# Kernel tuning notes

Measured on AMD Instinct MI355X. Metric: run time of the kernel, lower is better.

Reference implementation:

```python
import jax, jax.numpy as jnp
import numpy as np

EPS = 1e-5

def _conv3x3(x, w, b):
    # x: (B,C,H,W), w: (O,I,3,3) OIHW, SAME padding, stride 1
    y = jax.lax.conv_general_dilated(x, w, (1, 1), 'SAME',
                                     dimension_numbers=('NCHW', 'OIHW', 'NCHW'))
    return y + b[None, :, None, None]

def _inorm(x):
    # InstanceNorm2d (affine=False, eval-free): per-sample per-channel over HW
    m = jnp.mean(x, axis=(2, 3), keepdims=True)
    v = jnp.var(x, axis=(2, 3), keepdims=True)
    return (x - m) * jax.lax.rsqrt(v + EPS)

def _pac_conv_transpose(x, guide, w, b, stride=2, padding=1, out_pad=1):
    # PacConvTranspose2d (gaussian kernel, not channel-wise, unnormalized):
    # 1) zero-stuff input by stride, pad by (k-1)-padding (+output_padding on the
    #    bottom/right), 2) run a 3x3 conv whose taps are modulated per-pixel by
    #    K_ij = exp(-0.5 * ||g(p+ij) - g(p)||^2) computed from the guidance map.
    # w: (Cin, Cout, k, k)  (torch transposed-conv layout)
    k = w.shape[2]
    B, C, H, Wd = x.shape
    xs = jnp.zeros((B, C, (H - 1) * stride + 1, (Wd - 1) * stride + 1), x.dtype)
    xs = xs.at[:, :, ::stride, ::stride].set(x)
    p = (k - 1) - padding
    xp = jnp.pad(xs, ((0, 0), (0, 0), (p, p + out_pad), (p, p + out_pad)))
    gpad = (k - 1) // 2
    gp = jnp.pad(guide, ((0, 0), (0, 0), (gpad, gpad), (gpad, gpad)))
    Ho, Wo = guide.shape[2], guide.shape[3]
    out = jnp.zeros((B, w.shape[1], Ho, Wo), x.dtype)
    for i in range(k):          # fixed 3x3 tap loop (not a data-dim loop)
        for j in range(k):
            gn = gp[:, :, i:i + Ho, j:j + Wo]
            kk = jnp.exp(-0.5 * jnp.sum((gn - guide) ** 2, axis=1, keepdims=True))  # (B,1,Ho,Wo)
            xn = xp[:, :, i:i + Ho, j:j + Wo]                                        # (B,Cin,Ho,Wo)
            out = out + jnp.einsum('bchw,co->bohw', xn * kk, w[:, :, i, j])
    return out + b[None, :, None, None]

def setup_inputs() -> dict:
    key = jax.random.key(0)
    ks = jax.random.split(key, 16)
    C = 64
    s = 0.02  # small weight scale to keep gaussian adaptive kernels well-conditioned
    inp = {
        'x':      jax.random.normal(ks[0], (1, 4 * C, 64, 64), jnp.float32),
        'ef_lv2': jax.random.normal(ks[1], (1, 2 * C, 128, 128), jnp.float32),
        'ef_lv1': jax.random.normal(ks[2], (1, C, 256, 256), jnp.float32),
        'w_adj2': jax.random.normal(ks[3], (4 * C, 2 * C, 3, 3), jnp.float32) * s,
        'b_adj2': jnp.zeros((4 * C,), jnp.float32),
        'w_adj1': jax.random.normal(ks[4], (2 * C, C, 3, 3), jnp.float32) * s,
        'b_adj1': jnp.zeros((2 * C,), jnp.float32),
        'w_pac16': jax.random.normal(ks[5], (4 * C, 2 * C, 3, 3), jnp.float32) * s,
        'b_pac16': jnp.zeros((2 * C,), jnp.float32),
        'w_pac20': jax.random.normal(ks[6], (2 * C, C, 3, 3), jnp.float32) * s,
        'b_pac20': jnp.zeros((C,), jnp.float32),
        'w_out':  jax.random.normal(ks[7], (3, C, 3, 3), jnp.float32) * s,
        'b_out':  jnp.zeros((3,), jnp.float32),
    }
    return inp

def reference(x, ef_lv2, ef_lv1, w_adj2, b_adj2, w_adj1, b_adj1,
              w_pac16, b_pac16, w_pac20, b_pac20, w_out, b_out):
    x = _inorm(x) + x                       # layer13 + residual
    x = _inorm(x) + x                       # layer14 + residual
    g2 = _conv3x3(ef_lv2, w_adj2, b_adj2)   # adjust_ef_lv2_pacconv
    x = _pac_conv_transpose(x, g2, w_pac16, b_pac16)  # layer16: 64->128
    x = _inorm(x) + x                       # layer17
    x = _inorm(x) + x                       # layer18
    g1 = _conv3x3(ef_lv1, w_adj1, b_adj1)   # adjust_ef_lv1_pacconv
    x = _pac_conv_transpose(x, g1, w_pac20, b_pac20)  # layer20: 128->256
    x = _inorm(x) + x                       # layer21
    x = _inorm(x) + x                       # layer22
    return _conv3x3(x, w_out, b_out)        # layer24 -> (B,3,256,256)
```

## Files before the change

### kernel.cpp

```cpp
#include <hip/hip_runtime.h>
#include <hip/hip_bf16.h>
#include <cstdint>
#include <cstddef>

#define EPS_IN 1e-5f

typedef __attribute__((ext_vector_type(8))) short short8;
typedef __attribute__((ext_vector_type(4))) float floatx4;
typedef __attribute__((ext_vector_type(8))) unsigned short ushort8;
typedef __attribute__((ext_vector_type(4))) unsigned int uint4v;
typedef __attribute__((address_space(3))) unsigned int lds_uint;
typedef __attribute__((address_space(1))) const unsigned int glb_uint;

__device__ __forceinline__ unsigned short f2bf(float f) {
    unsigned int u = __float_as_uint(f);
    u += 0x7FFFu + ((u >> 16) & 1u);
    return (unsigned short)(u >> 16);
}
__device__ __forceinline__ float bf2f(unsigned short s) {
    return __uint_as_float((unsigned int)s << 16);
}
__device__ __forceinline__ float bflo(unsigned int u) {
    return __uint_as_float(u << 16);
}
__device__ __forceinline__ float bfhi(unsigned int u) {
    return __uint_as_float(u & 0xFFFF0000u);
}

__device__ __forceinline__ void composed_norm(float s, float q, float HW,
                                              float& A, float& B) {
    float m1 = s / HW;
    float v1 = q / HW - m1 * m1;
    float r1 = rsqrtf(v1 + EPS_IN);
    float a1 = 1.f + r1;
    float b1 = -m1 * r1;
    float r2 = rsqrtf(a1 * a1 * v1 + EPS_IN);
    float a2 = 1.f + r2;
    A = a1 * a2;
    B = a2 * b1 - m1 * r2;
}

__device__ __forceinline__ void border_zero(unsigned short* buf, int C, int H, int W, int idx) {
    int Hp = H + 2, Wp = W + 2;
    int cg8 = C >> 3;
    int cg = idx % cg8;
    int bi = idx / cg8;
    int y, x;
    if (bi < Wp) { y = 0; x = bi; }
    else if (bi < 2 * Wp) { y = Hp - 1; x = bi - Wp; }
    else {
        int k = bi - 2 * Wp;
        y = 1 + (k >> 1);
        x = (k & 1) ? (Wp - 1) : 0;
    }
    ushort8 z = {0, 0, 0, 0, 0, 0, 0, 0};
    *(ushort8*)&buf[((size_t)y * Wp + x) * C + cg * 8] = z;
}

__device__ __forceinline__ void reorder_one(const float* w, unsigned short* dst,
                                            int O, int C, int j) {
    int cg8 = C >> 3;
    int cg = j % cg8;
    int o = (j / cg8) % O;
    int tap = j / (cg8 * O);
    ushort8 v;
#pragma unroll
    for (int i = 0; i < 8; i++)
        v[i] = f2bf(w[((size_t)o * C + cg * 8 + i) * 9 + tap]);
    *(ushort8*)&dst[((size_t)tap * O + o) * C + cg * 8] = v;
}
__device__ __forceinline__ void stack_one(const float* w, unsigned short* dst,
                                          int C, int O, int j) {
    int cg8 = C >> 3;
    int cg = j % cg8;
    int o = (j / cg8) % O;
    int tap = j / (cg8 * O);
    ushort8 v;
#pragma unroll
    for (int i = 0; i < 8; i++)
        v[i] = f2bf(w[((size_t)(cg * 8 + i) * O + o) * 9 + tap]);
    *(ushort8*)&dst[((size_t)tap * O + o) * C + cg * 8] = v;
}

__device__ __forceinline__ void pad_one(const float* in, unsigned short* xp,
                                        int C, int H, int W, int t) {
    int HW = H * W;
    int p = t % HW;
    int cg = t / HW;
    int y = p / W, x = p % W;
    ushort8 v;
#pragma unroll
    for (int i = 0; i < 8; i++)
        v[i] = f2bf(in[(size_t)(cg * 8 + i) * HW + p]);
    *(ushort8*)&xp[((size_t)(y + 1) * (W + 2) + (x + 1)) * C + cg * 8] = v;
}

__global__ void prologue_kernel(uint4v* __restrict__ statz,
                                unsigned short* __restrict__ xp2,
                                unsigned short* __restrict__ xp1,
                                const float* __restrict__ w_adj2, unsigned short* __restrict__ Wr2,
                                const float* __restrict__ w_adj1, unsigned short* __restrict__ Wr1,
                                const float* __restrict__ w_p16, unsigned short* __restrict__ Wt16,
                                const float* __restrict__ w_p20, unsigned short* __restrict__ Wt20,
                                const float* __restrict__ ef2, const float* __restrict__ ef1,
                                const float* __restrict__ x, float2* __restrict__ statX) {
    __shared__ float ss[4], sq[4];
    int b = blockIdx.x;
    if (b < 68) {
        int t = b * 256 + threadIdx.x;
        const int NZ = 864;
        const int N2 = 516 * 16;
        const int N1 = 1028 * 8;
        if (t < NZ) {
            uint4v z = {0u, 0u, 0u, 0u};
            statz[t] = z;
        } else if (t < NZ + N2) {
            border_zero(xp2, 128, 128, 128, t - NZ);
        } else if (t < NZ + N2 + N1) {
            border_zero(xp1, 64, 256, 256, t - NZ - N2);
        }
    } else if (b < 428) {
        int t = (b - 68) * 256 + threadIdx.x;
        if (t < 36864) reorder_one(w_adj2, Wr2, 256, 128, t);
        else if (t < 46080) reorder_one(w_adj1, Wr1, 128, 64, t - 36864);
        else if (t < 82944) stack_one(w_p16, Wt16, 256, 128, t - 46080);
        else if (t < 92160) stack_one(w_p20, Wt20, 128, 64, t - 82944);
    } else if (b < 3500) {
        int t = (b - 428) * 256 + threadIdx.x;
        if (t < 262144) pad_one(ef2, xp2, 128, 128, 128, t);
        else            pad_one(ef1, xp1, 64, 256, 256, t - 262144);
    } else {
        int c = b - 3500;
        const float* src = x + (size_t)c * 4096;
        float s = 0.f, q = 0.f;
#pragma unroll
        for (int k = 0; k < 4; k++) {
            float4 v = *(const float4*)(src + k * 1024 + threadIdx.x * 4);
            s += v.x + v.y + v.z + v.w;
            q += v.x * v.x + v.y * v.y + v.z * v.z + v.w * v.w;
        }
#pragma unroll
        for (int off = 32; off >= 1; off >>= 1) {
            s += __shfl_down(s, off, 64);
            q += __shfl_down(q, off, 64);
        }
        int wave = threadIdx.x >> 6;
        if ((threadIdx.x & 63) == 0) { ss[wave] = s; sq[wave] = q; }
        __syncthreads();
        if (threadIdx.x == 0) {
            float2 o;
            o.x = ss[0] + ss[1] + ss[2] + ss[3];
            o.y = sq[0] + sq[1] + sq[2] + sq[3];
            statX[c] = o;
        }
    }
}

template <int CIN>
__device__ void conv3x3_body(const unsigned short* __restrict__ xp,
                             const unsigned short* __restrict__ wre,
                             const float* __restrict__ bias,
                             unsigned short* __restrict__ gpl,
                             int O, int H, int W, int bx) {
    __shared__ short Bbuf[390 * 32];
    __shared__ short Abuf[3 * 128 * 32];
    int tid = threadIdx.x;
    int lane = tid & 63, wid = tid >> 6;
    int mi = wid >> 1, ni = wid & 1;
    int l15 = lane & 15, khi = lane >> 4;
    int tpr = W >> 7;
    int y = bx / tpr;
    int x0 = (bx % tpr) << 7;
    int o0 = 0;
    int Wp = W + 2;
    int HW = H * W;

    floatx4 acc[4][4];
#pragma unroll
    for (int sm = 0; sm < 4; sm++)
#pragma unroll
        for (int r = 0; r < 4; r++) {
            float bv = bias[o0 + mi * 64 + sm * 16 + khi * 4 + r];
#pragma unroll
            for (int sn = 0; sn < 4; sn++) acc[sm][sn][r] = bv;
        }

    for (int cc = 0; cc < CIN / 32; cc++) {
        __syncthreads();
#pragma unroll
        for (int k = 0; k < 7; k++) {
            int s = k * 256 + tid;
            if (s < 1560) {
                int r = s >> 2, q = s & 3;
                int dy = r / 130, col = r % 130;
                const unsigned short* g =
                    xp + ((size_t)(y + dy) * Wp + x0 + col) * CIN + cc * 32 + q * 8;
                __builtin_amdgcn_global_load_lds((glb_uint*)g, (lds_uint*)(Bbuf + s * 8), 16, 0, 0);
            }
        }
        for (int dy = 0; dy < 3; dy++) {
            __syncthreads();
#pragma unroll
            for (int k = 0; k < 6; k++) {
                int s = k * 256 + tid;
                int dx = s >> 9, m = (s >> 2) & 127, q = s & 3;
                const unsigned short* g =
                    wre + ((size_t)((dy * 3 + dx) * O + o0 + m)) * CIN + cc * 32 + q * 8;
                __builtin_amdgcn_global_load_lds((glb_uint*)g, (lds_uint*)(Abuf + s * 8), 16, 0, 0);
            }
            __syncthreads();
#pragma unroll
            for (int dx = 0; dx < 3; dx++) {
                short8 a[4], b[4];
#pragma unroll
                for (int sm = 0; sm < 4; sm++)
                    a[sm] = *(const short8*)&Abuf[(dx * 128 + mi * 64 + sm * 16 + l15) * 32 + khi * 8];
#pragma unroll
                for (int sn = 0; sn < 4; sn++)
                    b[sn] = *(const short8*)&Bbuf[(dy * 130 + ni * 64 + sn * 16 + l15 + dx) * 32 + khi * 8];
#pragma unroll
                for (int sm = 0; sm < 4; sm++)
#pragma unroll
                    for (int sn = 0; sn < 4; sn++)
                        acc[sm][sn] = __builtin_amdgcn_mfma_f32_16x16x32_bf16(
                            a[sm], b[sn], acc[sm][sn], 0, 0, 0);
            }
        }
    }
#pragma unroll
    for (int sm = 0; sm < 4; sm++)
#pragma unroll
        for (int sn = 0; sn < 4; sn++) {
            int ob = o0 + mi * 64 + sm * 16 + khi * 4;
            int px = x0 + ni * 64 + sn * 16 + l15;
#pragma unroll
            for (int r = 0; r < 4; r++)
                gpl[(size_t)(ob + r) * HW + (size_t)y * W + px] = f2bf(acc[sm][sn][r]);
        }
}

template <int CIN>
__launch_bounds__(256, 1)
__global__ void conv3x3_mfma_at_kernel(const unsigned short* __restrict__ xp,
                                       const unsigned short* __restrict__ wre,
                                       const float* __restrict__ bias,
                                       unsigned short* __restrict__ gpl,
                                       int O, int H, int W) {
    __shared__ short Bbuf[390 * 32];
    __shared__ short Abuf[9 * 128 * 32];
    int tid = threadIdx.x;
    int lane = tid & 63, wid = tid >> 6;
    int mi = wid >> 1, ni = wid & 1;
    int l15 = lane & 15, khi = lane >> 4;
    int tpr = W >> 7;
    int y = blockIdx.x / tpr;
    int x0 = (blockIdx.x % tpr) << 7;
    int o0 = blockIdx.y << 7;
    int Wp = W + 2;
    int HW = H * W;

    floatx4 acc[4][4];
#pragma unroll
    for (int sm = 0; sm < 4; sm++)
#pragma unroll
        for (int r = 0; r < 4; r++) {
            float bv = bias[o0 + mi * 64 + sm * 16 + khi * 4 + r];
#pragma unroll
            for (int sn = 0; sn < 4; sn++) acc[sm][sn][r] = bv;
        }

    for (int cc = 0; cc < CIN / 32; cc++) {
        __syncthreads();
#pragma unroll
        for (int k = 0; k < 7; k++) {
            int s = k * 256 + tid;
            if (s < 1560) {
                int r = s >> 2, q = s & 3;
                int dy = r / 130, col = r % 130;
                const unsigned short* g =
                    xp + ((size_t)(y + dy) * Wp + x0 + col) * CIN + cc * 32 + q * 8;
                __builtin_amdgcn_global_load_lds((glb_uint*)g, (lds_uint*)(Bbuf + s * 8), 16, 0, 0);
            }
        }
#pragma unroll
        for (int k = 0; k < 18; k++) {
            int s = k * 256 + tid;
            int row = s >> 2, q = s & 3;
            int tap = row >> 7, m = row & 127;
            const unsigned short* g =
                wre + ((size_t)(tap * O + o0 + m)) * CIN + cc * 32 + q * 8;
            __builtin_amdgcn_global_load_lds((glb_uint*)g, (lds_uint*)(Abuf + s * 8), 16, 0, 0);
        }
        __syncthreads();
#pragma unroll
        for (int dy = 0; dy < 3; dy++)
#pragma unroll
            for (int dx = 0; dx < 3; dx++) {
                short8 a[4], b[4];
#pragma unroll
                for (int sm = 0; sm < 4; sm++)
                    a[sm] = *(const short8*)&Abuf[((dy * 3 + dx) * 128 + mi * 64 + sm * 16 + l15) * 32 + khi * 8];
#pragma unroll
                for (int sn = 0; sn < 4; sn++)
                    b[sn] = *(const short8*)&Bbuf[(dy * 130 + ni * 64 + sn * 16 + l15 + dx) * 32 + khi * 8];
#pragma unroll
                for (int sm = 0; sm < 4; sm++)
#pragma unroll
                    for (int sn = 0; sn < 4; sn++)
                        acc[sm][sn] = __builtin_amdgcn_mfma_f32_16x16x32_bf16(
                            a[sm], b[sn], acc[sm][sn], 0, 0, 0);
            }
    }
#pragma unroll
    for (int sm = 0; sm < 4; sm++)
#pragma unroll
        for (int sn = 0; sn < 4; sn++) {
            int ob = o0 + mi * 64 + sm * 16 + khi * 4;
            int px = x0 + ni * 64 + sn * 16 + l15;
#pragma unroll
            for (int r = 0; r < 4; r++)
                gpl[(size_t)(ob + r) * HW + (size_t)y * W + px] = f2bf(acc[sm][sn][r]);
        }
}

template <int CC>
__device__ __forceinline__ void kk_part_body(const unsigned short* __restrict__ g,
                                             float* __restrict__ S,
                                             int H, int W, int c0, int idx) {
    int Wh = W >> 1;
    int y = idx / Wh, xs = idx % Wh;
    int HW = H * W, HW4 = HW >> 2;
    int ys = y >> 1, ry = y & 1;
    bool xg = (xs + 1 < Wh);
    int off2 = xg ? 1 : 0;
    const unsigned short* gy = g + (size_t)y * W + 2 * xs + (size_t)c0 * HW;
    int slot = ys * Wh + xs;

    if (ry == 0) {
        float s3 = 0.f, s5 = 0.f;
        for (int c = 0; c < CC; c++) {
            const unsigned int* p = (const unsigned int*)(gy + (size_t)c * HW);
            unsigned int cc = p[0];
            unsigned int n2 = p[off2];
            float ce = bflo(cc), co = bfhi(cc);
            float d3 = ce - co;
            float d5 = bflo(n2) - co;
            s3 += d3 * d3;
            s5 += d5 * d5;
        }
        S[(size_t)3 * HW4 + slot] = s3;
        S[(size_t)4 * HW4 + slot] = 0.f;
        S[(size_t)5 * HW4 + slot] = xg ? s5 : 0.f;
    } else {
        bool yg = (y + 1 < H);
        float s0 = 0.f, s1 = 0.f, s2 = 0.f, s6 = 0.f, s7 = 0.f, s8 = 0.f;
        if (yg) {
            for (int c = 0; c < CC; c++) {
                const unsigned int* pc = (const unsigned int*)(gy + (size_t)c * HW);
                const unsigned int* pm = (const unsigned int*)(gy - W + (size_t)c * HW);
                const unsigned int* pp = (const unsigned int*)(gy + W + (size_t)c * HW);
                unsigned int cc = pc[0];
                unsigned int m0 = pm[0], m2 = pm[off2];
                unsigned int q0 = pp[0], q2 = pp[off2];
                float ce = bflo(cc), co = bfhi(cc);
                float nm = bflo(m0), np = bflo(q0);
                float d1 = nm - ce, d0 = nm - co, d2 = bflo(m2) - co;
                float d7 = np - ce, d6 = np - co, d8 = bflo(q2) - co;
                s1 += d1 * d1; s0 += d0 * d0; s2 += d2 * d2;
                s7 += d7 * d7; s6 += d6 * d6; s8 += d8 * d8;
            }
        } else {
            for (int c = 0; c < CC; c++) {
                const unsigned int* pc = (const unsigned int*)(gy + (size_t)c * HW);
                const unsigned int* pm = (const unsigned int*)(gy - W + (size_t)c * HW);
                unsigned int cc = pc[0];
                unsigned int m0 = pm[0], m2 = pm[off2];
                float ce = bflo(cc), co = bfhi(cc);
                float nm = bflo(m0);
                float d1 = nm - ce, d0 = nm - co, d2 = bflo(m2) - co;
                s1 += d1 * d1; s0 += d0 * d0; s2 += d2 * d2;
            }
        }
        S[(size_t)0 * HW4 + slot] = s0;
        S[(size_t)1 * HW4 + slot] = s1;
        S[(size_t)2 * HW4 + slot] = xg ? s2 : 0.f;
        S[(size_t)6 * HW4 + slot] = s6;
        S[(size_t)7 * HW4 + slot] = s7;
        S[(size_t)8 * HW4 + slot] = (xg && yg) ? s8 : 0.f;
    }
}

__launch_bounds__(256, 2)
__global__ void convg1_kk2_kernel(const unsigned short* __restrict__ Xp1,
                                  const unsigned short* __restrict__ Wr1,
                                  const float* __restrict__ b_adj1,
                                  unsigned short* __restrict__ Gp1,
                                  const unsigned short* __restrict__ Gp2,
                                  float* __restrict__ Sp2) {
    int b = blockIdx.x;
    if (b < 512) {
        conv3x3_body<64>(Xp1, Wr1, b_adj1, Gp1, 128, 256, 256, b);
    } else {
        b -= 512;
        int chunk = b >> 5, xblk = b & 31;
        kk_part_body<16>(Gp2, Sp2 + (size_t)chunk * 9 * 4096, 128, 128,
                         chunk * 16, xblk * 256 + (int)threadIdx.x);
    }
}

__global__ void kk1_red2_transpose_kernel(const unsigned short* __restrict__ Gp1,
                                          float* __restrict__ Sp1,
                                          const float* __restrict__ Sp2, float* __restrict__ Sf2,
                                          const float* __restrict__ x,
                                          const float2* __restrict__ statX,
                                          unsigned short* __restrict__ Xt16) {
    int b = blockIdx.x;
    if (b < 1024) {
        int chunk = b >> 7, xblk = b & 127;
        kk_part_body<16>(Gp1, Sp1 + (size_t)chunk * 9 * 16384, 256, 256,
                         chunk * 16, xblk * 256 + (int)threadIdx.x);
    } else if (b < 1168) {
        int i = (b - 1024) * 256 + threadIdx.x;
        if (i < 36864) {
            float s = 0.f;
            for (int ch = 0; ch < 16; ch++) s += Sp2[(size_t)ch * 36864 + i];
            Sf2[i] = s;
        }
    } else {
        int t = (b - 1168) * 256 + threadIdx.x;
        int p = t % 4096;
        int cg = t / 4096;
        float Av[8], Bv[8];
#pragma unroll
        for (int i = 0; i < 8; i++) {
            float2 pp = statX[cg * 8 + i];
            composed_norm(pp.x, pp.y, 4096.f, Av[i], Bv[i]);
        }
        ushort8 v;
#pragma unroll
        for (int i = 0; i < 8; i++) {
            float xv = x[(size_t)(cg * 8 + i) * 4096 + p];
            v[i] = f2bf(fmaf(xv, Av[i], Bv[i]));
        }
        *(ushort8*)&Xt16[(size_t)p * 256 + cg * 8] = v;
    }
}

template <int K>
__device__ void gemm_bt_body(const unsigned short* __restrict__ A,
                             const unsigned short* __restrict__ B,
                             unsigned short* __restrict__ P, int N,
                             int m0, int n0) {
    __shared__ short Ab[128 * 32];
    __shared__ short Bb[128 * 32];
    int tid = threadIdx.x;
    int lane = tid & 63, wid = tid >> 6;
    int mi = wid >> 1, ni = wid & 1;
    int l15 = lane & 15, khi = lane >> 4;

    floatx4 acc[4][4];
#pragma unroll
    for (int sm = 0; sm < 4; sm++)
#pragma unroll
        for (int sn = 0; sn < 4; sn++)
#pragma unroll
            for (int r = 0; r < 4; r++) acc[sm][sn][r] = 0.f;

    for (int kc = 0; kc < K / 32; kc++) {
        __syncthreads();
#pragma unroll
        for (int k = 0; k < 2; k++) {
            int s = k * 256 + tid;
            int row = s >> 2, q = s & 3;
            const unsigned short* ga = A + (size_t)(m0 + row) * K + kc * 32 + q * 8;
            __builtin_amdgcn_global_load_lds((glb_uint*)ga, (lds_uint*)(Ab + s * 8), 16, 0, 0);
            const unsigned short* gb = B + (size_t)(n0 + row) * K + kc * 32 + q * 8;
            __builtin_amdgcn_global_load_lds((glb_uint*)gb, (lds_uint*)(Bb + s * 8), 16, 0, 0);
        }
        __syncthreads();
        short8 a[4], b[4];
#pragma unroll
        for (int sm = 0; sm < 4; sm++)
            a[sm] = *(const short8*)&Ab[(mi * 64 + sm * 16 + l15) * 32 + khi * 8];
#pragma unroll
        for (int sn = 0; sn < 4; sn++)
            b[sn] = *(const short8*)&Bb[(ni * 64 + sn * 16 + l15) * 32 + khi * 8];
#pragma unroll
        for (int sm = 0; sm < 4; sm++)
#pragma unroll
            for (int sn = 0; sn < 4; sn++)
                acc[sm][sn] = __builtin_amdgcn_mfma_f32_16x16x32_bf16(
                    a[sm], b[sn], acc[sm][sn], 0, 0, 0);
    }
#pragma unroll
    for (int sm = 0; sm < 4; sm++)
#pragma unroll
        for (int sn = 0; sn < 4; sn++) {
            int m = m0 + mi * 64 + sm * 16 + khi * 4;
            int n = n0 + ni * 64 + sn * 16 + l15;
#pragma unroll
            for (int r = 0; r < 4; r++)
                P[(size_t)(m + r) * N + n] = f2bf(acc[sm][sn][r]);
        }
}

__launch_bounds__(256, 3)
__global__ void gemm16_red1_kernel(const unsigned short* __restrict__ Wt16,
                                   const unsigned short* __restrict__ Xt16,
                                   unsigned short* __restrict__ P16,
                                   const float* __restrict__ Sp1, float* __restrict__ Sf1) {
    int b = blockIdx.x;
    if (b < 288) {
        int n0 = (b & 31) << 7;
        int m0 = (b >> 5) << 7;
        gemm_bt_body<256>(Wt16, Xt16, P16, 4096, m0, n0);
    } else {
        int i = (b - 288) * 256 + threadIdx.x;
        if (i < 147456) {
            float s = 0.f;
            for (int ch = 0; ch < 8; ch++) s += Sp1[(size_t)ch * 147456 + i];
            Sf1[i] = s;
        }
    }
}

template <int K>
__launch_bounds__(256, 3)
__global__ void gemm_bt_kernel(const unsigned short* __restrict__ A,
                               const unsigned short* __restrict__ B,
                               unsigned short* __restrict__ P, int N) {
    gemm_bt_body<K>(A, B, P, N, blockIdx.y << 7, blockIdx.x << 7);
}

__global__ void transpose_norm2_bf16_kernel(const unsigned short* __restrict__ in,
                                            const float2* __restrict__ parts, int NB,
                                            unsigned short* __restrict__ xt,
                                            int C, int HW) {
    int t = blockIdx.x * blockDim.x + threadIdx.x;
    int p = t % HW;
    int cg = t / HW;
    float Av[8], Bv[8];
#pragma unroll
    for (int i = 0; i < 8; i++) {
        int c = cg * 8 + i;
        float s = 0.f, q = 0.f;
        for (int nb = 0; nb < NB; nb++) {
            float2 pp = parts[c * NB + nb];
            s += pp.x; q += pp.y;
        }
        composed_norm(s, q, (float)HW, Av[i], Bv[i]);
    }
    ushort8 v;
#pragma unroll
    for (int i = 0; i < 8; i++) {
        float x = bf2f(in[(size_t)(cg * 8 + i) * HW + p]);
        v[i] = f2bf(fmaf(x, Av[i], Bv[i]));
    }
    *(ushort8*)&xt[(size_t)p * C + cg * 8] = v;
}

__global__ void pac_combine2_kernel(const unsigned short* __restrict__ P,
                                    const float* __restrict__ S,
                                    const float* __restrict__ bias,
                                    unsigned short* __restrict__ out,
                                    float2* __restrict__ statOut,
                                    int O, int Hi, int Wi) {
    int HW4 = Hi * Wi;
    int Wo = Wi * 2;
    int HoWo = 4 * HW4;
    int idx = blockIdx.x * blockDim.x + threadIdx.x;
    int pixh = idx % HW4;
    int og = idx / HW4;
    int ys = pixh / Wi, xs = pixh % Wi;
    int ry = blockIdx.z;
    int y = 2 * ys + ry;
    bool xg = (xs + 1 < Wi);
    bool yg = (ys + 1 < Hi);
    size_t rowb = (size_t)ys * Wi + xs;

    float ev[4], ov[4];

    if (ry == 0) {
        float k3 = __expf(-0.5f * S[(size_t)3 * HW4 + pixh]);
        float k4 = __expf(-0.5f * S[(size_t)4 * HW4 + pixh]);
        float k5 = __expf(-0.5f * S[(size_t)5 * HW4 + pixh]);
#pragma unroll
        for (int r = 0; r < 4; r++) {
            int o = og * 4 + r;
            float bv = bias[o];
            const unsigned short* p3 = P + (size_t)(3 * O + o) * HW4 + rowb;
            const unsigned short* p4 = P + (size_t)(4 * O + o) * HW4 + rowb;
            const unsigned short* p5 = P + (size_t)(5 * O + o) * HW4 + rowb;
            float v4 = bf2f(p4[0]);
            float v3 = bf2f(p3[0]);
            float v5 = xg ? bf2f(p5[1]) : 0.f;
            ev[r] = bv + k4 * v4;
            ov[r] = bv + k3 * v3 + k5 * v5;
        }
    } else {
        float k0 = __expf(-0.5f * S[(size_t)0 * HW4 + pixh]);
        float k1 = __expf(-0.5f * S[(size_t)1 * HW4 + pixh]);
        float k2 = __expf(-0.5f * S[(size_t)2 * HW4 + pixh]);
        float k6 = __expf(-0.5f * S[(size_t)6 * HW4 + pixh]);
        float k7 = __expf(-0.5f * S[(size_t)7 * HW4 + pixh]);
        float k8 = __expf(-0.5f * S[(size_t)8 * HW4 + pixh]);
#pragma unroll
        for (int r = 0; r < 4; r++) {
            int o = og * 4 + r;
            float bv = bias[o];
            const unsigned short* p0 = P + (size_t)(0 * O + o) * HW4 + rowb;
            const unsigned short* p1 = P + (size_t)(1 * O + o) * HW4 + rowb;
            const unsigned short* p2 = P + (size_t)(2 * O + o) * HW4 + rowb;
            const unsigned short* p6 = P + (size_t)(6 * O + o) * HW4 + rowb + Wi;
            const unsigned short* p7 = P + (size_t)(7 * O + o) * HW4 + rowb + Wi;
            const unsigned short* p8 = P + (size_t)(8 * O + o) * HW4 + rowb + Wi;
            float v1 = bf2f(p1[0]);
            float v0 = bf2f(p0[0]);
            float v2 = xg ? bf2f(p2[1]) : 0.f;
            float v7 = yg ? bf2f(p7[0]) : 0.f;
            float v6 = yg ? bf2f(p6[0]) : 0.f;
            float v8 = (yg && xg) ? bf2f(p8[1]) : 0.f;
            ev[r] = bv + k1 * v1 + k7 * v7;
            ov[r] = bv + k0 * v0 + k2 * v2 + k6 * v6 + k8 * v8;
        }
    }
#pragma unroll
    for (int r = 0; r < 4; r++) {
        unsigned int pk = (unsigned int)f2bf(ev[r]) | ((unsigned int)f2bf(ov[r]) << 16);
        *(unsigned int*)&out[(size_t)(og * 4 + r) * HoWo + (size_t)y * Wo + 2 * xs] = pk;
    }

    __shared__ float rs[4][4], rq[4][4];
    int wave = threadIdx.x >> 6;
#pragma unroll
    for (int r = 0; r < 4; r++) {
        float s = ev[r] + ov[r];
        float q = ev[r] * ev[r] + ov[r] * ov[r];
#pragma unroll
        for (int off = 32; off >= 1; off >>= 1) {
            s += __shfl_down(s, off, 64);
            q += __shfl_down(q, off, 64);
        }
        if ((threadIdx.x & 63) == 0) { rs[wave][r] = s; rq[wave][r] = q; }
    }
    __syncthreads();
    if (threadIdx.x < 4) {
        int r = threadIdx.x;
        float s = rs[0][r] + rs[1][r] + rs[2][r] + rs[3][r];
        float q = rq[0][r] + rq[1][r] + rq[2][r] + rq[3][r];
        atomicAdd(&statOut[og * 4 + r].x, s);
        atomicAdd(&statOut[og * 4 + r].y, q);
    }
}

__global__ void conv_part_norm_kernel(const unsigned short* __restrict__ in,
                                      const float* __restrict__ w,
                                      const float2* __restrict__ parts, int NB,
                                      float* __restrict__ Pf, int H, int W) {
    __shared__ float wsm[16 * 9 * 3];
    __shared__ float am[16], bm[16];
    int q0 = blockIdx.y * 16;
    int HW = H * W;
    for (int t = threadIdx.x; t < 432; t += blockDim.x) {
        int oc = t % 3;
        int tap = (t / 3) % 9;
        int c = t / 27;
        wsm[t] = w[((size_t)oc * 64 + q0 + c) * 9 + tap];
    }
    if (threadIdx.x < 16) {
        int c = q0 + threadIdx.x;
        float s = 0.f, q = 0.f;
        for (int nb = 0; nb < NB; nb++) {
            float2 pp = parts[c * NB + nb];
            s += pp.x; q += pp.y;
        }
        float A, B;
        composed_norm(s, q, (float)HW, A, B);
        am[threadIdx.x] = A;
        bm[threadIdx.x] = B;
    }
    __syncthreads();
    int pix = blockIdx.x * blockDim.x + threadIdx.x;
    int y = pix / W, x = pix % W;
    float acc[3] = {0.f, 0.f, 0.f};
    bool xl = (x > 0), xr = (x < W - 1);
    for (int c = 0; c < 16; c++) {
        const unsigned short* base = in + (size_t)(q0 + c) * HW + pix;
        const float* wc = wsm + c * 27;
        float ac = am[c], bc = bm[c];
#pragma unroll
        for (int dy = 0; dy < 3; dy++) {
            int yy = y + dy - 1;
            if (yy < 0 || yy >= H) continue;
            const unsigned short* row = base + (dy - 1) * W;
            float v0 = xl ? fmaf(bf2f(row[-1]), ac, bc) : 0.f;
            float v1 = fmaf(bf2f(row[0]), ac, bc);
            float v2 = xr ? fmaf(bf2f(row[1]), ac, bc) : 0.f;
#pragma unroll
            for (int ob = 0; ob < 3; ob++) {
                acc[ob] += v0 * wc[(dy * 3 + 0) * 3 + ob];
                acc[ob] += v1 * wc[(dy * 3 + 1) * 3 + ob];
                acc[ob] += v2 * wc[(dy * 3 + 2) * 3 + ob];
            }
        }
    }
#pragma unroll
    for (int ob = 0; ob < 3; ob++)
        Pf[(size_t)(blockIdx.y * 3 + ob) * HW + pix] = acc[ob];
}

__global__ void conv_fin_kernel(const float* __restrict__ Pf, const float* __restrict__ bias,
                                float* __restrict__ out, int HW) {
    int pix = blockIdx.x * blockDim.x + threadIdx.x;
#pragma unroll
    for (int ob = 0; ob < 3; ob++) {
        float a = bias[ob];
#pragma unroll
        for (int q = 0; q < 4; q++)
            a += Pf[(size_t)(q * 3 + ob) * HW + pix];
        out[(size_t)ob * HW + pix] = a;
    }
}

extern "C" void kernel_launch(void* const* d_in, const int* in_sizes, int n_in,
                              void* d_out, int out_size, void* d_ws, size_t ws_size,
                              hipStream_t stream) {
    const float* x      = (const float*)d_in[0];
    const float* ef2    = (const float*)d_in[1];
    const float* ef1    = (const float*)d_in[2];
    const float* w_adj2 = (const float*)d_in[3];
    const float* b_adj2 = (const float*)d_in[4];
    const float* w_adj1 = (const float*)d_in[5];
    const float* b_adj1 = (const float*)d_in[6];
    const float* w_p16  = (const float*)d_in[7];
    const float* b_p16  = (const float*)d_in[8];
    const float* w_p20  = (const float*)d_in[9];
    const float* b_p20  = (const float*)d_in[10];
    const float* w_out  = (const float*)d_in[11];
    const float* b_out  = (const float*)d_in[12];
    float* out = (float*)d_out;

    float* ws = (float*)d_ws;
    unsigned short* bxb1 = (unsigned short*)(ws + 1048576);
    unsigned short* bxb2 = (unsigned short*)(ws + 3145728);
    unsigned short* Wt16 = (unsigned short*)(ws + 5242880);
    unsigned short* Xt16 = (unsigned short*)(ws + 5390336);
    float* bk2c = ws + 7340032;
    float* bk1c = ws + 7376896;
    float2* statX   = (float2*)(ws + 7524352);
    float2* statP16 = (float2*)(ws + 7525376);
    float2* statP20 = (float2*)(ws + 7526656);
    unsigned short* Wt20 = (unsigned short*)(ws + 7528832);
    unsigned short* Gp1  = (unsigned short*)(ws + 7569792);
    unsigned short* P16  = (unsigned short*)(ws + 7569792);
    unsigned short* P20  = (unsigned short*)(ws + 7569792);
    unsigned short* Gp2  = (unsigned short*)(ws + 12812672);
    unsigned short* Xt20 = (unsigned short*)(ws + 12812672);
    unsigned short* Xp2 = (unsigned short*)(ws + 14975872);
    unsigned short* Wr2 = (unsigned short*)(ws + 16057472);
    unsigned short* Xp1 = (unsigned short*)(ws + 16204928);
    unsigned short* Wr1 = (unsigned short*)(ws + 18334976);
    float* Pf = ws + 14975872;
    float* Sp2 = ws + 18371840;
    float* Sp1 = ws + 18961664;

    prologue_kernel<<<3756, 256, 0, stream>>>(
        (uint4v*)(ws + 7525376), Xp2, Xp1,
        w_adj2, Wr2, w_adj1, Wr1, w_p16, Wt16, w_p20, Wt20,
        ef2, ef1, x, statX);

    conv3x3_mfma_at_kernel<128><<<dim3(128, 2), 256, 0, stream>>>(Xp2, Wr2, b_adj2, Gp2, 256, 128, 128);

    convg1_kk2_kernel<<<1024, 256, 0, stream>>>(Xp1, Wr1, b_adj1, Gp1, Gp2, Sp2);

    kk1_red2_transpose_kernel<<<1680, 256, 0, stream>>>(Gp1, Sp1, Sp2, bk2c, x, statX, Xt16);

    gemm16_red1_kernel<<<864, 256, 0, stream>>>(Wt16, Xt16, P16, Sp1, bk1c);

    pac_combine2_kernel<<<dim3(512, 1, 2), 256, 0, stream>>>(P16, bk2c, b_p16, bxb1, statP16, 128, 64, 64);

    transpose_norm2_bf16_kernel<<<1024, 256, 0, stream>>>(bxb1, statP16, 1, Xt20, 128, 16384);

    gemm_bt_kernel<128><<<dim3(128, 5), 256, 0, stream>>>(Wt20, Xt20, P20, 16384);

    pac_combine2_kernel<<<dim3(1024, 1, 2), 256, 0, stream>>>(P20, bk1c, b_p20, bxb2, statP20, 64, 128, 128);

    conv_part_norm_kernel<<<dim3(256, 4), 256, 0, stream>>>(bxb2, w_out, statP20, 1, Pf, 256, 256);
    conv_fin_kernel<<<256, 256, 0, stream>>>(Pf, b_out, out, 65536);
}
```

Baseline: 234.1 us.

## Run g1 guide conv with the all-taps conv kernel and regroup the kk and reduction stages

```diff
diff --git a/kernel.cpp b/kernel.cpp
--- a/kernel.cpp
+++ b/kernel.cpp
@@ -154,89 +154,6 @@
             statX[c] = o;
         }
     }
-}
-
-template <int CIN>
-__device__ void conv3x3_body(const unsigned short* __restrict__ xp,
-                             const unsigned short* __restrict__ wre,
-                             const float* __restrict__ bias,
-                             unsigned short* __restrict__ gpl,
-                             int O, int H, int W, int bx) {
-    __shared__ short Bbuf[390 * 32];
-    __shared__ short Abuf[3 * 128 * 32];
-    int tid = threadIdx.x;
-    int lane = tid & 63, wid = tid >> 6;
-    int mi = wid >> 1, ni = wid & 1;
-    int l15 = lane & 15, khi = lane >> 4;
-    int tpr = W >> 7;
-    int y = bx / tpr;
-    int x0 = (bx % tpr) << 7;
-    int o0 = 0;
-    int Wp = W + 2;
-    int HW = H * W;
-
-    floatx4 acc[4][4];
-#pragma unroll
-    for (int sm = 0; sm < 4; sm++)
-#pragma unroll
-        for (int r = 0; r < 4; r++) {
-            float bv = bias[o0 + mi * 64 + sm * 16 + khi * 4 + r];
-#pragma unroll
-            for (int sn = 0; sn < 4; sn++) acc[sm][sn][r] = bv;
-        }
-
-    for (int cc = 0; cc < CIN / 32; cc++) {
-        __syncthreads();
-#pragma unroll
-        for (int k = 0; k < 7; k++) {
-            int s = k * 256 + tid;
-            if (s < 1560) {
-                int r = s >> 2, q = s & 3;
-                int dy = r / 130, col = r % 130;
-                const unsigned short* g =
-                    xp + ((size_t)(y + dy) * Wp + x0 + col) * CIN + cc * 32 + q * 8;
-                __builtin_amdgcn_global_load_lds((glb_uint*)g, (lds_uint*)(Bbuf + s * 8), 16, 0, 0);
-            }
-        }
-        for (int dy = 0; dy < 3; dy++) {
-            __syncthreads();
-#pragma unroll
-            for (int k = 0; k < 6; k++) {
-                int s = k * 256 + tid;
-                int dx = s >> 9, m = (s >> 2) & 127, q = s & 3;
-                const unsigned short* g =
-                    wre + ((size_t)((dy * 3 + dx) * O + o0 + m)) * CIN + cc * 32 + q * 8;
-                __builtin_amdgcn_global_load_lds((glb_uint*)g, (lds_uint*)(Abuf + s * 8), 16, 0, 0);
-            }
-            __syncthreads();
-#pragma unroll
-            for (int dx = 0; dx < 3; dx++) {
-                short8 a[4], b[4];
-#pragma unroll
-                for (int sm = 0; sm < 4; sm++)
-                    a[sm] = *(const short8*)&Abuf[(dx * 128 + mi * 64 + sm * 16 + l15) * 32 + khi * 8];
-#pragma unroll
-                for (int sn = 0; sn < 4; sn++)
-                    b[sn] = *(const short8*)&Bbuf[(dy * 130 + ni * 64 + sn * 16 + l15 + dx) * 32 + khi * 8];
-#pragma unroll
-                for (int sm = 0; sm < 4; sm++)
-#pragma unroll
-                    for (int sn = 0; sn < 4; sn++)
-                        acc[sm][sn] = __builtin_amdgcn_mfma_f32_16x16x32_bf16(
-                            a[sm], b[sn], acc[sm][sn], 0, 0, 0);
-            }
-        }
-    }
-#pragma unroll
-    for (int sm = 0; sm < 4; sm++)
-#pragma unroll
-        for (int sn = 0; sn < 4; sn++) {
-            int ob = o0 + mi * 64 + sm * 16 + khi * 4;
-            int px = x0 + ni * 64 + sn * 16 + l15;
-#pragma unroll
-            for (int r = 0; r < 4; r++)
-                gpl[(size_t)(ob + r) * HW + (size_t)y * W + px] = f2bf(acc[sm][sn][r]);
-        }
 }
 
 template <int CIN>
@@ -390,44 +307,25 @@
     }
 }
 
-__launch_bounds__(256, 2)
-__global__ void convg1_kk2_kernel(const unsigned short* __restrict__ Xp1,
-                                  const unsigned short* __restrict__ Wr1,
-                                  const float* __restrict__ b_adj1,
-                                  unsigned short* __restrict__ Gp1,
-                                  const unsigned short* __restrict__ Gp2,
-                                  float* __restrict__ Sp2) {
+__global__ void kk_both_transpose_kernel(const unsigned short* __restrict__ Gp2,
+                                         float* __restrict__ Sp2,
+                                         const unsigned short* __restrict__ Gp1,
+                                         float* __restrict__ Sp1,
+                                         const float* __restrict__ x,
+                                         const float2* __restrict__ statX,
+                                         unsigned short* __restrict__ Xt16) {
     int b = blockIdx.x;
     if (b < 512) {
-        conv3x3_body<64>(Xp1, Wr1, b_adj1, Gp1, 128, 256, 256, b);
-    } else {
-        b -= 512;
         int chunk = b >> 5, xblk = b & 31;
         kk_part_body<16>(Gp2, Sp2 + (size_t)chunk * 9 * 4096, 128, 128,
                          chunk * 16, xblk * 256 + (int)threadIdx.x);
-    }
-}
-
-__global__ void kk1_red2_transpose_kernel(const unsigned short* __restrict__ Gp1,
-                                          float* __restrict__ Sp1,
-                                          const float* __restrict__ Sp2, float* __restrict__ Sf2,
-                                          const float* __restrict__ x,
-                                          const float2* __restrict__ statX,
-                                          unsigned short* __restrict__ Xt16) {
-    int b = blockIdx.x;
-    if (b < 1024) {
+    } else if (b < 1536) {
+        b -= 512;
         int chunk = b >> 7, xblk = b & 127;
         kk_part_body<16>(Gp1, Sp1 + (size_t)chunk * 9 * 16384, 256, 256,
                          chunk * 16, xblk * 256 + (int)threadIdx.x);
-    } else if (b < 1168) {
-        int i = (b - 1024) * 256 + threadIdx.x;
-        if (i < 36864) {
-            float s = 0.f;
-            for (int ch = 0; ch < 16; ch++) s += Sp2[(size_t)ch * 36864 + i];
-            Sf2[i] = s;
-        }
     } else {
-        int t = (b - 1168) * 256 + threadIdx.x;
+        int t = (b - 1536) * 256 + threadIdx.x;
         int p = t % 4096;
         int cg = t / 4096;
         float Av[8], Bv[8];
@@ -505,17 +403,25 @@
 }
 
 __launch_bounds__(256, 3)
-__global__ void gemm16_red1_kernel(const unsigned short* __restrict__ Wt16,
-                                   const unsigned short* __restrict__ Xt16,
-                                   unsigned short* __restrict__ P16,
-                                   const float* __restrict__ Sp1, float* __restrict__ Sf1) {
+__global__ void gemm16_red_kernel(const unsigned short* __restrict__ Wt16,
+                                  const unsigned short* __restrict__ Xt16,
+                                  unsigned short* __restrict__ P16,
+                                  const float* __restrict__ Sp2, float* __restrict__ Sf2,
+                                  const float* __restrict__ Sp1, float* __restrict__ Sf1) {
     int b = blockIdx.x;
     if (b < 288) {
         int n0 = (b & 31) << 7;
         int m0 = (b >> 5) << 7;
         gemm_bt_body<256>(Wt16, Xt16, P16, 4096, m0, n0);
+    } else if (b < 432) {
+        int i = (b - 288) * 256 + threadIdx.x;
+        if (i < 36864) {
+            float s = 0.f;
+            for (int ch = 0; ch < 16; ch++) s += Sp2[(size_t)ch * 36864 + i];
+            Sf2[i] = s;
+        }
     } else {
-        int i = (b - 288) * 256 + threadIdx.x;
+        int i = (b - 432) * 256 + threadIdx.x;
         if (i < 147456) {
             float s = 0.f;
             for (int ch = 0; ch < 8; ch++) s += Sp1[(size_t)ch * 147456 + i];
@@ -771,11 +677,11 @@
 
     conv3x3_mfma_at_kernel<128><<<dim3(128, 2), 256, 0, stream>>>(Xp2, Wr2, b_adj2, Gp2, 256, 128, 128);
 
-    convg1_kk2_kernel<<<1024, 256, 0, stream>>>(Xp1, Wr1, b_adj1, Gp1, Gp2, Sp2);
-
-    kk1_red2_transpose_kernel<<<1680, 256, 0, stream>>>(Gp1, Sp1, Sp2, bk2c, x, statX, Xt16);
-
-    gemm16_red1_kernel<<<864, 256, 0, stream>>>(Wt16, Xt16, P16, Sp1, bk1c);
+    conv3x3_mfma_at_kernel<64><<<dim3(512, 1), 256, 0, stream>>>(Xp1, Wr1, b_adj1, Gp1, 128, 256, 256);
+
+    kk_both_transpose_kernel<<<2048, 256, 0, stream>>>(Gp2, Sp2, Gp1, Sp1, x, statX, Xt16);
+
+    gemm16_red_kernel<<<1008, 256, 0, stream>>>(Wt16, Xt16, P16, Sp2, bk2c, Sp1, bk1c);
 
     pac_combine2_kernel<<<dim3(512, 1, 2), 256, 0, stream>>>(P16, bk2c, b_p16, bxb1, statP16, 128, 64, 64);
 
```

After: 233.4 us. Within noise of the previous version (-0.3%).
